# Optimization experiments

Hardware: AMD Instinct MI355X
Metric: run time of the kernel (lower is better)

## Reference

```python
import jax, jax.numpy as jnp
import numpy as np

DIM, HEADS, WS, SS = 256, 8, 4, 2
B, D, H, W = 2, 16, 56, 56


def _rel_pos_index(ws):
    coords = np.stack(np.meshgrid(np.arange(ws), np.arange(ws), np.arange(ws), indexing='ij'))
    flat = coords.reshape(3, -1)                      # [3, n]
    rel = (flat[:, :, None] - flat[:, None, :]).transpose(1, 2, 0).astype(np.int64)  # [n,n,3]
    rel[..., 0] += ws - 1; rel[..., 1] += ws - 1; rel[..., 2] += ws - 1
    rel[..., 0] *= (2 * ws - 1) ** 2
    rel[..., 1] *= (2 * ws - 1)
    return rel.sum(-1)                                # [n, n]


def _attn_mask(d, h, w, ws, ss):
    # dims are divisible by ws here, so padded dims == dims (matches torch ceil-pad)
    img = np.zeros((d, h, w))
    sl = (slice(0, -ws), slice(-ws, -ss), slice(-ss, None))
    cnt = 0
    for dsl in sl:
        for hsl in sl:
            for wsl in sl:
                img[dsl, hsl, wsl] = cnt
                cnt += 1
    mw = img.reshape(d // ws, ws, h // ws, ws, w // ws, ws)
    mw = mw.transpose(0, 2, 4, 1, 3, 5).reshape(-1, ws ** 3)   # [nW, n]
    diff = mw[:, None, :] - mw[:, :, None]
    return np.where(diff != 0, -100.0, 0.0).astype(np.float32)  # [nW, n, n]


def _window_partition(x, ws):
    b, d, h, w, c = x.shape
    x = x.reshape(b, d // ws, ws, h // ws, ws, w // ws, ws, c)
    return x.transpose(0, 1, 3, 5, 2, 4, 6, 7).reshape(-1, ws ** 3, c)


def _window_reverse(win, ws, b, d, h, w, c):
    x = win.reshape(b, d // ws, h // ws, w // ws, ws, ws, ws, c)
    return x.transpose(0, 1, 4, 2, 5, 3, 6, 7).reshape(b, d, h, w, c)


def _ln(x, g, b, eps=1e-5):
    mu = x.mean(-1, keepdims=True)
    var = ((x - mu) ** 2).mean(-1, keepdims=True)
    return (x - mu) * jax.lax.rsqrt(var + eps) * g + b


def setup_inputs() -> dict:
    key = jax.random.key(0)
    ks = jax.random.split(key, 8)
    s = 0.02
    return {
        'x': jax.random.normal(ks[0], (B, D, H, W, DIM), jnp.float32),
        'norm1_g': jnp.ones((DIM,), jnp.float32),
        'norm1_b': jnp.zeros((DIM,), jnp.float32),
        'qkv_w': jax.random.normal(ks[1], (DIM, 3 * DIM), jnp.float32) * s,
        'qkv_b': jnp.zeros((3 * DIM,), jnp.float32),
        'proj_w': jax.random.normal(ks[2], (DIM, DIM), jnp.float32) * s,
        'proj_b': jnp.zeros((DIM,), jnp.float32),
        'rpb_table': jax.random.normal(ks[3], ((2 * WS - 1) ** 3, HEADS), jnp.float32) * s,
        'norm2_g': jnp.ones((DIM,), jnp.float32),
        'norm2_b': jnp.zeros((DIM,), jnp.float32),
        'fc1_w': jax.random.normal(ks[4], (DIM, 4 * DIM), jnp.float32) * s,
        'fc1_b': jnp.zeros((4 * DIM,), jnp.float32),
        'fc2_w': jax.random.normal(ks[5], (4 * DIM, DIM), jnp.float32) * s,
        'fc2_b': jnp.zeros((DIM,), jnp.float32),
    }


def reference(x, norm1_g, norm1_b, qkv_w, qkv_b, proj_w, proj_b, rpb_table,
              norm2_g, norm2_b, fc1_w, fc1_b, fc2_w, fc2_b):
    b, d, h, w, c = x.shape
    nh, ws, ss = HEADS, WS, SS
    hd = c // nh
    shortcut = x

    xn = _ln(x, norm1_g, norm1_b)
    xs = jnp.roll(xn, shift=(-ss, -ss, -ss), axis=(1, 2, 3))
    xw = _window_partition(xs, ws)            # [B_, n, c]
    B_, n, _ = xw.shape

    qkv = (xw @ qkv_w + qkv_b).reshape(B_, n, 3, nh, hd).transpose(2, 0, 3, 1, 4)
    q, k, v = qkv[0], qkv[1], qkv[2]          # [B_, nh, n, hd]
    attn = jnp.einsum('bhqd,bhkd->bhqk', q * (hd ** -0.5), k)

    rpi = jnp.asarray(_rel_pos_index(ws).reshape(-1))
    bias = rpb_table[rpi].reshape(n, n, nh).transpose(2, 0, 1)  # [nh, n, n]
    attn = attn + bias[None]

    mask = jnp.asarray(_attn_mask(d, h, w, ws, ss))             # [nW, n, n]
    nW = mask.shape[0]
    attn = attn.reshape(B_ // nW, nW, nh, n, n) + mask[None, :, None]
    attn = jax.nn.softmax(attn.reshape(B_, nh, n, n), axis=-1)

    out = jnp.einsum('bhqk,bhkd->bhqd', attn, v).transpose(0, 2, 1, 3).reshape(B_, n, c)
    out = out @ proj_w + proj_b

    xr = _window_reverse(out, ws, b, d, h, w, c)
    xr = jnp.roll(xr, shift=(ss, ss, ss), axis=(1, 2, 3))
    x1 = shortcut + xr

    y = _ln(x1, norm2_g, norm2_b)
    y = jax.nn.gelu(y @ fc1_w + fc1_b, approximate=False) @ fc2_w + fc2_b
    return x1 + y
```

## Files before the change

kernel.cpp:

```cpp
#include <hip/hip_runtime.h>
#include <math.h>


using f32x4  = __attribute__((ext_vector_type(4))) float;
using bf16x8 = __attribute__((ext_vector_type(8))) short;

__device__ __forceinline__ short f2bf(float f) {
  unsigned u = __builtin_bit_cast(unsigned, f);
  u += 0x7fffu + ((u >> 16) & 1u);
  return (short)(u >> 16);
}

__device__ __forceinline__ float gelu_f(float v) {
  const float u = 1.5957691216057308f * v * (1.f + 0.044715f * v * v);
  const float e = __expf(u);
  return v - v * __builtin_amdgcn_rcpf(e + 1.f);
}

#define GLDS16(g, l) __builtin_amdgcn_global_load_lds(                        \
    (__attribute__((address_space(1))) void*)(g),                             \
    (__attribute__((address_space(3))) void*)(l), 16, 0, 0)

__global__ void transpose_all_k(const float* __restrict__ qkv_w,
                                const float* __restrict__ proj_w,
                                const float* __restrict__ fc1_w,
                                const float* __restrict__ fc2_w,
                                short* __restrict__ o_qkv,
                                short* __restrict__ o_proj,
                                short* __restrict__ o_fc1,
                                short* __restrict__ o_fc2) {
  int bid = blockIdx.x;
  const float* in; short* out; int K, N;
  if (bid < 768)       { in = qkv_w;  out = o_qkv;  K = 256;  N = 768; }
  else if (bid < 1024) { in = proj_w; out = o_proj; K = 256;  N = 256;  bid -= 768; }
  else if (bid < 2048) { in = fc1_w;  out = o_fc1;  K = 256;  N = 1024; bid -= 1024; }
  else                 { in = fc2_w;  out = o_fc2;  K = 1024; N = 256;  bid -= 2048; }
  const int idx = bid * 256 + threadIdx.x;
  const int k = idx / N, n = idx % N;
  out[(size_t)n * K + k] = f2bf(in[idx]);
}

__global__ __launch_bounds__(256) void ln1_part_k(
    const float* __restrict__ x, const float* __restrict__ g,
    const float* __restrict__ bta, short* __restrict__ xw) {
  const int wave = threadIdx.x >> 6, lane = threadIdx.x & 63;
  const int row = blockIdx.x * 4 + wave;
  const int win = row >> 6, tok = row & 63;
  const int b = win / 784, wi = win % 784;
  const int wd = wi / 196, wh = (wi / 14) % 14, ww = wi % 14;
  const int tz = tok >> 4, ty = (tok >> 2) & 3, tx = tok & 3;
  const int gd = (wd * 4 + tz + 2) & 15;
  int gh = wh * 4 + ty + 2; if (gh >= 56) gh -= 56;
  int gw = ww * 4 + tx + 2; if (gw >= 56) gw -= 56;
  const size_t src = ((((size_t)b * 16 + gd) * 56 + gh) * 56 + gw) * 256;
  const float4 v = ((const float4*)(x + src))[lane];
  float s = v.x + v.y + v.z + v.w;
#pragma unroll
  for (int m = 1; m < 64; m <<= 1) s += __shfl_xor(s, m);
  const float mean = s * (1.f / 256.f);
  const float dx = v.x - mean, dy = v.y - mean, dz = v.z - mean, dw = v.w - mean;
  float q = dx * dx + dy * dy + dz * dz + dw * dw;
#pragma unroll
  for (int m = 1; m < 64; m <<= 1) q += __shfl_xor(q, m);
  const float rstd = rsqrtf(q * (1.f / 256.f) + 1e-5f);
  const float4 gg = ((const float4*)g)[lane];
  const float4 bb = ((const float4*)bta)[lane];
  short4 o;
  o.x = f2bf(dx * rstd * gg.x + bb.x);
  o.y = f2bf(dy * rstd * gg.y + bb.y);
  o.z = f2bf(dz * rstd * gg.z + bb.z);
  o.w = f2bf(dw * rstd * gg.w + bb.w);
  *(short4*)(xw + (size_t)row * 256 + lane * 4) = o;
}

__global__ __launch_bounds__(256) void ln2_k(
    const float* __restrict__ x1, const float* __restrict__ g,
    const float* __restrict__ bta, short* __restrict__ yn) {
  const int wave = threadIdx.x >> 6, lane = threadIdx.x & 63;
  const int row = blockIdx.x * 4 + wave;
  const float4 v = ((const float4*)(x1 + (size_t)row * 256))[lane];
  float s = v.x + v.y + v.z + v.w;
#pragma unroll
  for (int m = 1; m < 64; m <<= 1) s += __shfl_xor(s, m);
  const float mean = s * (1.f / 256.f);
  const float dx = v.x - mean, dy = v.y - mean, dz = v.z - mean, dw = v.w - mean;
  float q = dx * dx + dy * dy + dz * dz + dw * dw;
#pragma unroll
  for (int m = 1; m < 64; m <<= 1) q += __shfl_xor(q, m);
  const float rstd = rsqrtf(q * (1.f / 256.f) + 1e-5f);
  const float4 gg = ((const float4*)g)[lane];
  const float4 bb = ((const float4*)bta)[lane];
  short4 o;
  o.x = f2bf(dx * rstd * gg.x + bb.x);
  o.y = f2bf(dy * rstd * gg.y + bb.y);
  o.z = f2bf(dz * rstd * gg.z + bb.z);
  o.w = f2bf(dw * rstd * gg.w + bb.w);
  *(short4*)(yn + (size_t)row * 256 + lane * 4) = o;
}

template <int EPI>
__global__ __launch_bounds__(256) void gemm_k(
    const short* __restrict__ A, const short* __restrict__ Bt,
    const float* __restrict__ bias, const float* __restrict__ resid,
    void* __restrict__ OutP, int N, int K) {
  __shared__ short SMEM[16384];
  short* As = SMEM;
  short* Bs = SMEM + 8192;
  const int tid = threadIdx.x;
  const int wave = tid >> 6, lane = tid & 63;
  const int quad = lane >> 4, l15 = lane & 15;
  const int m0 = blockIdx.y * 128;
  const int n0 = blockIdx.x * 128;
  const int wm = (wave >> 1) * 64, wn = (wave & 1) * 64;

  f32x4 acc[4][4] = {};

  for (int k0 = 0; k0 < K; k0 += 64) {
    __syncthreads();
#pragma unroll
    for (int i = 0; i < 4; ++i) {
      const int p = wave * 256 + i * 64 + lane;
      const int row = p >> 3;
      const int c = (p & 7) ^ (row & 7);
      GLDS16(A  + (size_t)(m0 + row) * K + (k0 + c * 8),
             As + (size_t)(wave * 256 + i * 64) * 8);
      GLDS16(Bt + (size_t)(n0 + row) * K + (k0 + c * 8),
             Bs + (size_t)(wave * 256 + i * 64) * 8);
    }
    __syncthreads();
#pragma unroll
    for (int ks = 0; ks < 2; ++ks) {
      bf16x8 af[4], bfr[4];
#pragma unroll
      for (int t = 0; t < 4; ++t) {
        const int ra = wm + t * 16 + l15;
        const int ca = (ks * 4 + quad) ^ (ra & 7);
        af[t] = *(const bf16x8*)(As + ra * 64 + ca * 8);
        const int rb = wn + t * 16 + l15;
        const int cb = (ks * 4 + quad) ^ (rb & 7);
        bfr[t] = *(const bf16x8*)(Bs + rb * 64 + cb * 8);
      }
#pragma unroll
      for (int mt = 0; mt < 4; ++mt)
#pragma unroll
        for (int nt = 0; nt < 4; ++nt)
          acc[mt][nt] = __builtin_amdgcn_mfma_f32_16x16x32_bf16(
              af[mt], bfr[nt], acc[mt][nt], 0, 0, 0);
    }
  }

  __syncthreads();
  if constexpr (EPI == 0 || EPI == 1) {
#pragma unroll
    for (int nt = 0; nt < 4; ++nt) {
      const int col = wn + nt * 16 + l15;
      const float bv = bias[n0 + col];
#pragma unroll
      for (int mt = 0; mt < 4; ++mt)
#pragma unroll
        for (int reg = 0; reg < 4; ++reg) {
          const int row = wm + mt * 16 + quad * 4 + reg;
          float v = acc[mt][nt][reg] + bv;
          if constexpr (EPI == 1) v = gelu_f(v);
          const int byte = (row << 8) | ((col << 1) ^ ((row & 7) << 4));
          *(short*)((char*)SMEM + byte) = f2bf(v);
        }
    }
    __syncthreads();
    short* out = (short*)OutP;
#pragma unroll
    for (int i = 0; i < 8; ++i) {
      const int off = i * 4096 + tid * 16;
      const int row = off >> 8;
      const bf16x8 val =
          *(const bf16x8*)((char*)SMEM + (off ^ ((row & 7) << 4)));
      *(bf16x8*)(out + (size_t)(m0 + row) * N + n0 + ((off & 255) >> 1)) = val;
    }
  } else {
    float* out = (float*)OutP;
#pragma unroll
    for (int hh = 0; hh < 2; ++hh) {
      if (hh) __syncthreads();
      if (wm == hh * 64) {
#pragma unroll
        for (int nt = 0; nt < 4; ++nt) {
          const int col = wn + nt * 16 + l15;
          const float bv = bias[n0 + col];
#pragma unroll
          for (int mt = 0; mt < 4; ++mt)
#pragma unroll
            for (int reg = 0; reg < 4; ++reg) {
              const int rloc = mt * 16 + quad * 4 + reg;
              const int byte = (rloc << 9) | ((col << 2) ^ ((rloc & 7) << 4));
              *(float*)((char*)SMEM + byte) = acc[mt][nt][reg] + bv;
            }
        }
      }
      __syncthreads();
#pragma unroll
      for (int i = 0; i < 8; ++i) {
        const int off = i * 4096 + tid * 16;
        const int rloc = off >> 9;
        f32x4 val = *(const f32x4*)((char*)SMEM + (off ^ ((rloc & 7) << 4)));
        const int colf = (off & 511) >> 2;
        const int grow = m0 + hh * 64 + rloc;
        size_t dst;
        if constexpr (EPI == 2) {
          const int win = grow >> 6, tok = grow & 63;
          const int b = win / 784, wi = win % 784;
          const int wd = wi / 196, wh = (wi / 14) % 14, ww = wi % 14;
          const int tz = tok >> 4, ty = (tok >> 2) & 3, tx = tok & 3;
          const int gd = (wd * 4 + tz + 2) & 15;
          int gh = wh * 4 + ty + 2; if (gh >= 56) gh -= 56;
          int gw = ww * 4 + tx + 2; if (gw >= 56) gw -= 56;
          dst = ((((size_t)b * 16 + gd) * 56 + gh) * 56 + gw) * 256
                + n0 + colf;
        } else {
          dst = (size_t)grow * 256 + n0 + colf;
        }
        const f32x4 r = *(const f32x4*)(resid + dst);
        val = val + r;
        *(f32x4*)(out + dst) = val;
      }
    }
  }
}

__global__ __launch_bounds__(256) void attn_k(
    const short* __restrict__ qkv, const float* __restrict__ rpb,
    short* __restrict__ aout) {
  __shared__ short Plds[4 * 64 * 80];
  const int tid = threadIdx.x;
  const int wave = tid >> 6, lane = tid & 63;
  const int quad = lane >> 4, l15 = lane & 15;
  const int win = blockIdx.x >> 1;
  const int h = ((blockIdx.x & 1) << 2) + wave;
  const int wi = win % 784;
  const int wd = wi / 196, wh = (wi / 14) % 14, ww = wi % 14;
  const short* base = qkv + (size_t)win * (64 * 768);

  bf16x8 qf[4], kf[4];
#pragma unroll
  for (int t = 0; t < 4; ++t) {
    const short* qp = base + (size_t)(t * 16 + l15) * 768 + h * 32 + quad * 8;
    qf[t] = *(const bf16x8*)qp;
    kf[t] = *(const bf16x8*)(qp + 256);
  }
  f32x4 S[4][4] = {};
#pragma unroll
  for (int mt = 0; mt < 4; ++mt)
#pragma unroll
    for (int nt = 0; nt < 4; ++nt)
      S[mt][nt] = __builtin_amdgcn_mfma_f32_16x16x32_bf16(
          qf[mt], kf[nt], S[mt][nt], 0, 0, 0);

  const bool bd = (wd == 3), bh = (wh == 13), bw = (ww == 13);
  const int yc = l15 >> 2, xc = l15 & 3;
  int labc[4];
#pragma unroll
  for (int nt = 0; nt < 4; ++nt) {
    const int rd = bd ? (nt < 2 ? 1 : 2) : 0;
    const int rh = bh ? (yc < 2 ? 1 : 2) : 0;
    const int rw = bw ? (xc < 2 ? 1 : 2) : 0;
    labc[nt] = rd * 9 + rh * 3 + rw;
  }
  const float scale = 0.17677669529663687f;
#pragma unroll
  for (int mt = 0; mt < 4; ++mt) {
    const int rdr = bd ? (mt < 2 ? 1 : 2) : 0;
    const int rhr = bh ? (quad < 2 ? 1 : 2) : 0;
#pragma unroll
    for (int reg = 0; reg < 4; ++reg) {
      const int rwr = bw ? (reg < 2 ? 1 : 2) : 0;
      const int labr = rdr * 9 + rhr * 3 + rwr;
      float sc[4];
#pragma unroll
      for (int nt = 0; nt < 4; ++nt) {
        const int rpi = (mt - nt + 3) * 49 + (quad - yc + 3) * 7 + (reg - xc + 3);
        const float bias = rpb[rpi * 8 + h];
        const float mv = (labr == labc[nt]) ? 0.f : -100.f;
        sc[nt] = S[mt][nt][reg] * scale + bias + mv;
      }
      float mx = fmaxf(fmaxf(sc[0], sc[1]), fmaxf(sc[2], sc[3]));
      mx = fmaxf(mx, __shfl_xor(mx, 1));
      mx = fmaxf(mx, __shfl_xor(mx, 2));
      mx = fmaxf(mx, __shfl_xor(mx, 4));
      mx = fmaxf(mx, __shfl_xor(mx, 8));
      float p[4], sum = 0.f;
#pragma unroll
      for (int nt = 0; nt < 4; ++nt) { p[nt] = __expf(sc[nt] - mx); sum += p[nt]; }
      sum += __shfl_xor(sum, 1);
      sum += __shfl_xor(sum, 2);
      sum += __shfl_xor(sum, 4);
      sum += __shfl_xor(sum, 8);
      const float inv = 1.f / sum;
      const int r = mt * 16 + quad * 4 + reg;
#pragma unroll
      for (int nt = 0; nt < 4; ++nt)
        Plds[(wave * 64 + r) * 80 + nt * 16 + l15] = f2bf(p[nt] * inv);
    }
  }

  bf16x8 vf[2][2];
#pragma unroll
  for (int kt = 0; kt < 2; ++kt)
#pragma unroll
    for (int n2 = 0; n2 < 2; ++n2)
#pragma unroll
      for (int j = 0; j < 8; ++j)
        vf[kt][n2][j] =
            base[(size_t)(kt * 32 + quad * 8 + j) * 768 + 512 + h * 32 + n2 * 16 + l15];

  f32x4 O[4][2] = {};
#pragma unroll
  for (int mt = 0; mt < 4; ++mt) {
    const short* pr = &Plds[(wave * 64 + mt * 16 + l15) * 80 + quad * 8];
    const bf16x8 pa0 = *(const bf16x8*)pr;
    const bf16x8 pa1 = *(const bf16x8*)(pr + 32);
#pragma unroll
    for (int n2 = 0; n2 < 2; ++n2) {
      O[mt][n2] = __builtin_amdgcn_mfma_f32_16x16x32_bf16(pa0, vf[0][n2], O[mt][n2], 0, 0, 0);
      O[mt][n2] = __builtin_amdgcn_mfma_f32_16x16x32_bf16(pa1, vf[1][n2], O[mt][n2], 0, 0, 0);
    }
  }
#pragma unroll
  for (int mt = 0; mt < 4; ++mt)
#pragma unroll
    for (int n2 = 0; n2 < 2; ++n2)
#pragma unroll
      for (int reg = 0; reg < 4; ++reg) {
        const int tok = mt * 16 + quad * 4 + reg;
        aout[((size_t)win * 64 + tok) * 256 + h * 32 + n2 * 16 + l15] =
            f2bf(O[mt][n2][reg]);
      }
}

extern "C" void kernel_launch(void* const* d_in, const int* in_sizes, int n_in,
                              void* d_out, int out_size, void* d_ws,
                              size_t ws_size, hipStream_t stream) {
  const float* x      = (const float*)d_in[0];
  const float* n1g    = (const float*)d_in[1];
  const float* n1b    = (const float*)d_in[2];
  const float* qkv_w  = (const float*)d_in[3];
  const float* qkv_b  = (const float*)d_in[4];
  const float* proj_w = (const float*)d_in[5];
  const float* proj_b = (const float*)d_in[6];
  const float* rpb    = (const float*)d_in[7];
  const float* n2g    = (const float*)d_in[8];
  const float* n2b    = (const float*)d_in[9];
  const float* fc1_w  = (const float*)d_in[10];
  const float* fc1_b  = (const float*)d_in[11];
  const float* fc2_w  = (const float*)d_in[12];
  const float* fc2_b  = (const float*)d_in[13];

  char* ws = (char*)d_ws;
  short* wt_qkv  = (short*)(ws + 0);
  short* wt_proj = (short*)(ws + 393216);
  short* wt_fc1  = (short*)(ws + 524288);
  short* wt_fc2  = (short*)(ws + 1048576);
  short* bufS    = (short*)(ws + 1572864);
  short* bufL    = (short*)(ws + 52953088);
  float* x1      = (float*)d_out;

  transpose_all_k<<<3072, 256, 0, stream>>>(qkv_w, proj_w, fc1_w, fc2_w,
                                            wt_qkv, wt_proj, wt_fc1, wt_fc2);
  ln1_part_k<<<25088, 256, 0, stream>>>(x, n1g, n1b, bufS);
  gemm_k<0><<<dim3(6, 784), 256, 0, stream>>>(bufS, wt_qkv, qkv_b, nullptr,
                                              bufL, 768, 256);
  attn_k<<<3136, 256, 0, stream>>>(bufL, rpb, bufS);
  gemm_k<2><<<dim3(2, 784), 256, 0, stream>>>(bufS, wt_proj, proj_b, x,
                                              x1, 256, 256);
  ln2_k<<<25088, 256, 0, stream>>>(x1, n2g, n2b, bufS);
  gemm_k<1><<<dim3(8, 784), 256, 0, stream>>>(bufS, wt_fc1, fc1_b, nullptr,
                                              bufL, 1024, 256);
  gemm_k<3><<<dim3(2, 784), 256, 0, stream>>>(bufL, wt_fc2, fc2_b, x1,
                                              x1, 256, 1024);
}
```

Measured before the change: 705.9 us.

## Fuse fc1, GELU and fc2 into a single MLP kernel

Replaces the separate fc1+GELU GEMM and fc2 GEMM with one kernel that handles 64 tokens per block. It loops over 128-wide hidden chunks, keeps the GELU output in LDS, and accumulates the fc2 result in registers. This avoids writing the 1024-wide hidden activation to global memory and reading it back. In exchange, each block reloads A tiles eight times, fetches W2 fragments directly from global without LDS staging, and runs only 1568 blocks with a sequential loop over hidden chunks. The gemm_k epilogue is simplified now that the EPI==1 and EPI==3 paths are gone.

Measured after the change: 766.3 us. 1.09x slower.

```diff
diff --git a/kernel.cpp b/kernel.cpp
--- a/kernel.cpp
+++ b/kernel.cpp
@@ -4,6 +4,8 @@
 
 using f32x4  = __attribute__((ext_vector_type(4))) float;
 using bf16x8 = __attribute__((ext_vector_type(8))) short;
+
+#define MFMA16 __builtin_amdgcn_mfma_f32_16x16x32_bf16
 
 __device__ __forceinline__ short f2bf(float f) {
   unsigned u = __builtin_bit_cast(unsigned, f);
@@ -144,13 +146,12 @@
       for (int mt = 0; mt < 4; ++mt)
 #pragma unroll
         for (int nt = 0; nt < 4; ++nt)
-          acc[mt][nt] = __builtin_amdgcn_mfma_f32_16x16x32_bf16(
-              af[mt], bfr[nt], acc[mt][nt], 0, 0, 0);
+          acc[mt][nt] = MFMA16(af[mt], bfr[nt], acc[mt][nt], 0, 0, 0);
     }
   }
 
   __syncthreads();
-  if constexpr (EPI == 0 || EPI == 1) {
+  if constexpr (EPI == 0) {
 #pragma unroll
     for (int nt = 0; nt < 4; ++nt) {
       const int col = wn + nt * 16 + l15;
@@ -160,10 +161,8 @@
 #pragma unroll
         for (int reg = 0; reg < 4; ++reg) {
           const int row = wm + mt * 16 + quad * 4 + reg;
-          float v = acc[mt][nt][reg] + bv;
-          if constexpr (EPI == 1) v = gelu_f(v);
           const int byte = (row << 8) | ((col << 1) ^ ((row & 7) << 4));
-          *(short*)((char*)SMEM + byte) = f2bf(v);
+          *(short*)((char*)SMEM + byte) = f2bf(acc[mt][nt][reg] + bv);
         }
     }
     __syncthreads();
@@ -204,24 +203,158 @@
         f32x4 val = *(const f32x4*)((char*)SMEM + (off ^ ((rloc & 7) << 4)));
         const int colf = (off & 511) >> 2;
         const int grow = m0 + hh * 64 + rloc;
-        size_t dst;
-        if constexpr (EPI == 2) {
-          const int win = grow >> 6, tok = grow & 63;
-          const int b = win / 784, wi = win % 784;
-          const int wd = wi / 196, wh = (wi / 14) % 14, ww = wi % 14;
-          const int tz = tok >> 4, ty = (tok >> 2) & 3, tx = tok & 3;
-          const int gd = (wd * 4 + tz + 2) & 15;
-          int gh = wh * 4 + ty + 2; if (gh >= 56) gh -= 56;
-          int gw = ww * 4 + tx + 2; if (gw >= 56) gw -= 56;
-          dst = ((((size_t)b * 16 + gd) * 56 + gh) * 56 + gw) * 256
-                + n0 + colf;
-        } else {
-          dst = (size_t)grow * 256 + n0 + colf;
-        }
+        const int win = grow >> 6, tok = grow & 63;
+        const int b = win / 784, wi = win % 784;
+        const int wd = wi / 196, wh = (wi / 14) % 14, ww = wi % 14;
+        const int tz = tok >> 4, ty = (tok >> 2) & 3, tx = tok & 3;
+        const int gd = (wd * 4 + tz + 2) & 15;
+        int gh = wh * 4 + ty + 2; if (gh >= 56) gh -= 56;
+        int gw = ww * 4 + tx + 2; if (gw >= 56) gw -= 56;
+        const size_t dst = ((((size_t)b * 16 + gd) * 56 + gh) * 56 + gw) * 256
+                           + n0 + colf;
         const f32x4 r = *(const f32x4*)(resid + dst);
         val = val + r;
         *(f32x4*)(out + dst) = val;
       }
+    }
+  }
+}
+
+__global__ __launch_bounds__(256) void mlp_k(
+    const short* __restrict__ A,
+    const short* __restrict__ W1,
+    const short* __restrict__ W2,
+    const float* __restrict__ b1, const float* __restrict__ b2,
+    const float* __restrict__ resid,
+    float* __restrict__ out) {
+  __shared__ short SMEM[20480];
+  short* As = SMEM;
+  short* Bs = SMEM + 4096;
+  short* Hs = SMEM + 12288;
+  const int tid = threadIdx.x;
+  const int wave = tid >> 6, lane = tid & 63;
+  const int quad = lane >> 4, l15 = lane & 15;
+  const int wr = wave >> 1, wc = wave & 1;
+  const int m0 = blockIdx.x * 64;
+
+  f32x4 oacc[4][4] = {};
+
+  for (int j = 0; j < 8; ++j) {
+    f32x4 hacc[2][4] = {};
+    for (int k0 = 0; k0 < 256; k0 += 64) {
+      __syncthreads();
+#pragma unroll
+      for (int i = 0; i < 2; ++i) {
+        const int p = i * 256 + tid;
+        const int row = p >> 3;
+        const int c = (p & 7) ^ (row & 7);
+        GLDS16(A + (size_t)(m0 + row) * 256 + (k0 + c * 8),
+               As + (size_t)p * 8);
+      }
+#pragma unroll
+      for (int i = 0; i < 4; ++i) {
+        const int p = i * 256 + tid;
+        const int row = p >> 3;
+        const int c = (p & 7) ^ (row & 7);
+        GLDS16(W1 + (size_t)(j * 128 + row) * 256 + (k0 + c * 8),
+               Bs + (size_t)p * 8);
+      }
+      __syncthreads();
+#pragma unroll
+      for (int ks = 0; ks < 2; ++ks) {
+        bf16x8 af[2], bfr[4];
+#pragma unroll
+        for (int mt = 0; mt < 2; ++mt) {
+          const int ra = wr * 32 + mt * 16 + l15;
+          const int ca = (ks * 4 + quad) ^ (ra & 7);
+          af[mt] = *(const bf16x8*)(As + ra * 64 + ca * 8);
+        }
+#pragma unroll
+        for (int nt = 0; nt < 4; ++nt) {
+          const int rb = wc * 64 + nt * 16 + l15;
+          const int cb = (ks * 4 + quad) ^ (rb & 7);
+          bfr[nt] = *(const bf16x8*)(Bs + rb * 64 + cb * 8);
+        }
+#pragma unroll
+        for (int mt = 0; mt < 2; ++mt)
+#pragma unroll
+          for (int nt = 0; nt < 4; ++nt)
+            hacc[mt][nt] = MFMA16(af[mt], bfr[nt], hacc[mt][nt], 0, 0, 0);
+      }
+    }
+#pragma unroll
+    for (int nt = 0; nt < 4; ++nt) {
+      const int h = wc * 64 + nt * 16 + l15;
+      const float bv = b1[j * 128 + h];
+      const int hc = h >> 3, hsub = (h & 7) * 2;
+#pragma unroll
+      for (int mt = 0; mt < 2; ++mt)
+#pragma unroll
+        for (int reg = 0; reg < 4; ++reg) {
+          const int t = wr * 32 + mt * 16 + quad * 4 + reg;
+          const float v = gelu_f(hacc[mt][nt][reg] + bv);
+          const int byte = t * 256 + ((hc ^ (t & 7)) << 4) + hsub;
+          *(short*)((char*)Hs + byte) = f2bf(v);
+        }
+    }
+    bf16x8 bf2[4][4];
+#pragma unroll
+    for (int kk = 0; kk < 4; ++kk)
+#pragma unroll
+      for (int nt = 0; nt < 4; ++nt) {
+        const int n = wave * 64 + nt * 16 + l15;
+        bf2[kk][nt] = *(const bf16x8*)(
+            W2 + (size_t)n * 1024 + j * 128 + kk * 32 + quad * 8);
+      }
+    __syncthreads();
+#pragma unroll
+    for (int kk = 0; kk < 4; ++kk) {
+      bf16x8 af2[4];
+#pragma unroll
+      for (int mt = 0; mt < 4; ++mt) {
+        const int t = mt * 16 + l15;
+        const int c = kk * 4 + quad;
+        af2[mt] = *(const bf16x8*)((char*)Hs + t * 256 + ((c ^ (t & 7)) << 4));
+      }
+#pragma unroll
+      for (int mt = 0; mt < 4; ++mt)
+#pragma unroll
+        for (int nt = 0; nt < 4; ++nt)
+          oacc[mt][nt] = MFMA16(af2[mt], bf2[kk][nt], oacc[mt][nt], 0, 0, 0);
+    }
+  }
+
+#pragma unroll
+  for (int hh = 0; hh < 2; ++hh) {
+    __syncthreads();
+#pragma unroll
+    for (int mi = 0; mi < 2; ++mi) {
+      const int mt = hh * 2 + mi;
+#pragma unroll
+      for (int nt = 0; nt < 4; ++nt) {
+        const int col = wave * 64 + nt * 16 + l15;
+        const float bv = b2[col];
+#pragma unroll
+        for (int reg = 0; reg < 4; ++reg) {
+          const int rl = mi * 16 + quad * 4 + reg;
+          const int byte =
+              rl * 1024 + (((col >> 2) ^ (rl & 7)) << 4) + (col & 3) * 4;
+          *(float*)((char*)SMEM + byte) = oacc[mt][nt][reg] + bv;
+        }
+      }
+    }
+    __syncthreads();
+#pragma unroll
+    for (int i = 0; i < 8; ++i) {
+      const int off = i * 4096 + tid * 16;
+      const int rloc = off >> 10;
+      const int win = off & 1023;
+      const int byte = rloc * 1024 + (((win >> 4) ^ (rloc & 7)) << 4);
+      f32x4 v = *(const f32x4*)((char*)SMEM + byte);
+      const size_t dst = (size_t)(m0 + hh * 32 + rloc) * 256 + (win >> 2);
+      const f32x4 r = *(const f32x4*)(resid + dst);
+      v = v + r;
+      *(f32x4*)(out + dst) = v;
     }
   }
 }
@@ -251,8 +384,7 @@
   for (int mt = 0; mt < 4; ++mt)
 #pragma unroll
     for (int nt = 0; nt < 4; ++nt)
-      S[mt][nt] = __builtin_amdgcn_mfma_f32_16x16x32_bf16(
-          qf[mt], kf[nt], S[mt][nt], 0, 0, 0);
+      S[mt][nt] = MFMA16(qf[mt], kf[nt], S[mt][nt], 0, 0, 0);
 
   const bool bd = (wd == 3), bh = (wh == 13), bw = (ww == 13);
   const int yc = l15 >> 2, xc = l15 & 3;
@@ -319,8 +451,8 @@
     const bf16x8 pa1 = *(const bf16x8*)(pr + 32);
 #pragma unroll
     for (int n2 = 0; n2 < 2; ++n2) {
-      O[mt][n2] = __builtin_amdgcn_mfma_f32_16x16x32_bf16(pa0, vf[0][n2], O[mt][n2], 0, 0, 0);
-      O[mt][n2] = __builtin_amdgcn_mfma_f32_16x16x32_bf16(pa1, vf[1][n2], O[mt][n2], 0, 0, 0);
+      O[mt][n2] = MFMA16(pa0, vf[0][n2], O[mt][n2], 0, 0, 0);
+      O[mt][n2] = MFMA16(pa1, vf[1][n2], O[mt][n2], 0, 0, 0);
     }
   }
 #pragma unroll
@@ -371,8 +503,6 @@
   gemm_k<2><<<dim3(2, 784), 256, 0, stream>>>(bufS, wt_proj, proj_b, x,
                                               x1, 256, 256);
   ln2_k<<<25088, 256, 0, stream>>>(x1, n2g, n2b, bufS);
-  gemm_k<1><<<dim3(8, 784), 256, 0, stream>>>(bufS, wt_fc1, fc1_b, nullptr,
-                                              bufL, 1024, 256);
-  gemm_k<3><<<dim3(2, 784), 256, 0, stream>>>(bufL, wt_fc2, fc2_b, x1,
-                                              x1, 256, 1024);
-}
+  mlp_k<<<1568, 256, 0, stream>>>(bufS, wt_fc1, wt_fc2, fc1_b, fc2_b,
+                                  x1, x1);
+}
```
